# Kernel optimization log

Hardware: AMD Instinct MI355X
Metric: run time of the kernel (lower is better)

The kernel has to match this reference:

```python
import jax, jax.numpy as jnp
import numpy as np

EPS = 1e-5
GROUPS = 4
KSZ = 3
PAD = 1
CUTON = 0.1


def conv1x1(x, w):
    # x: [b,c,h,w], w: [o,c,1,1]
    return jnp.einsum('bchw,oc->bohw', x, w[:, :, 0, 0])


def bn_eval(x, g, b, m, v):
    scale = g / jnp.sqrt(v + EPS)
    return (x - m[None, :, None, None]) * scale[None, :, None, None] + b[None, :, None, None]


def extract_patches(xp, k):
    # xp: [b,c,H+2p,W+2p] -> [b,c,h,w,k,k] (matches torch unfold(2,k,1).unfold(3,k,1))
    h = xp.shape[2] - k + 1
    w = xp.shape[3] - k + 1
    p = jnp.stack([xp[:, :, i:i + h, j:j + w] for i in range(k) for j in range(k)], axis=-1)
    return p.reshape(p.shape[:-1] + (k, k))


def batch_fftshift(z):
    # faithful to roll_n with n = d//2 (+1 if odd), over dims 1..3; roll_n == roll by -n
    for ax in (1, 2, 3):
        d = z.shape[ax]
        z = jnp.roll(z, -(d // 2 + (d % 2)), axis=ax)
    return z


def batch_ifftshift(z):
    for ax in (3, 2, 1):
        z = jnp.roll(z, -(z.shape[ax] // 2), axis=ax)
    return z


def attention_conv(x, yq, q_w, k_w, v_w, rel_h, rel_w):
    b, c, h, w = x.shape
    C = q_w.shape[0]
    px = jnp.pad(x, ((0, 0), (0, 0), (PAD, PAD), (PAD, PAD)))
    q = conv1x1(yq, q_w)                      # [b,C,h,w]
    k = conv1x1(px, k_w)
    v = conv1x1(px, v_w)
    kp = extract_patches(k, KSZ)              # [b,C,h,w,3,3]
    vp = extract_patches(v, KSZ)
    kh, kw = kp[:, :C // 2], kp[:, C // 2:]
    kp = jnp.concatenate([kh + rel_h, kw + rel_w], axis=1)
    kp = kp.reshape(b, GROUPS, C // GROUPS, h, w, KSZ * KSZ)
    vp = vp.reshape(b, GROUPS, C // GROUPS, h, w, KSZ * KSZ)
    q = q.reshape(b, GROUPS, C // GROUPS, h, w, 1)
    attn = jax.nn.softmax(q * kp, axis=-1)
    out = jnp.einsum('bgchwk,bgchwk->bgchw', attn, vp)
    return out.reshape(b, C, h, w)


def fam(x, rate1, rate2, w1, w0_w, w0_b):
    h, w = x.shape[2], x.shape[3]
    # torch.fft.fftn with dim=None -> FFT over ALL dims (batch & channel too)
    x_ft = jnp.fft.fftn(x, norm='ortho')
    out_ft = jnp.einsum('bixy,ioxy->boxy', x_ft, w1)
    s = batch_fftshift(out_ft)
    cy, cx = h // 2, w // 2
    rh, rw = int(CUTON * cy), int(CUTON * cx)
    mask = jnp.ones((h, w), dtype=x.dtype).at[cy - rh:cy + rh, cx - rw:cx + rw].set(0.0)
    s = s * mask
    out_ft = batch_ifftshift(s)
    # torch.fft.ifftn with s=(h,w) -> inverse FFT over last two dims only
    out = jnp.fft.ifftn(out_ft, s=(h, w), norm='ortho').real
    out2 = conv1x1(x, w0_w) + w0_b[None, :, None, None]
    return rate1 * out + rate2 * out2


def setup_inputs() -> dict:
    key = jax.random.key(0)
    ks = jax.random.split(key, 16)
    B, Cx, Cy, M, O, H, W = 4, 128, 256, 128, 128, 64, 64
    scale = 1.0 / (M * O)
    inp = {
        'x': jax.random.normal(ks[0], (B, Cx, H, W), jnp.float32),
        'y': jax.random.normal(ks[1], (B, Cy, H // 2, W // 2), jnp.float32),
        'conv1_w': jax.random.normal(ks[2], (M, Cy, 1, 1), jnp.float32) * 0.05,
        'bn1_g': jnp.ones((M,), jnp.float32),
        'bn1_b': jnp.zeros((M,), jnp.float32),
        'bn1_m': jnp.zeros((M,), jnp.float32),
        'bn1_v': jnp.ones((M,), jnp.float32),
        'q_w': jax.random.normal(ks[3], (M, M, 1, 1), jnp.float32) * 0.05,
        'k_w': jax.random.normal(ks[4], (M, M, 1, 1), jnp.float32) * 0.05,
        'v_w': jax.random.normal(ks[5], (M, M, 1, 1), jnp.float32) * 0.05,
        'rel_h': jax.random.normal(ks[6], (M // 2, 1, 1, 3, 1), jnp.float32),
        'rel_w': jax.random.normal(ks[7], (M // 2, 1, 1, 1, 3), jnp.float32),
        'rate1': jnp.full((1,), 0.5, jnp.float32),
        'rate2': jnp.full((1,), 0.5, jnp.float32),
        'w1_real': scale * jax.random.uniform(ks[8], (M, O, H, W), jnp.float32),
        'w1_imag': scale * jax.random.uniform(ks[9], (M, O, H, W), jnp.float32),
        'w0_w': jax.random.normal(ks[10], (O, M, 1, 1), jnp.float32) * 0.05,
        'w0_b': jnp.zeros((O,), jnp.float32),
        'bn2_g': jnp.ones((O,), jnp.float32),
        'bn2_b': jnp.zeros((O,), jnp.float32),
        'bn2_m': jnp.zeros((O,), jnp.float32),
        'bn2_v': jnp.ones((O,), jnp.float32),
    }
    return inp


def reference(x, y, conv1_w, bn1_g, bn1_b, bn1_m, bn1_v, q_w, k_w, v_w, rel_h, rel_w,
              rate1, rate2, w1_real, w1_imag, w0_w, w0_b, bn2_g, bn2_b, bn2_m, bn2_v):
    # conv1 (teacher proj) + BN + ReLU
    y1 = jax.nn.relu(bn_eval(conv1x1(y, conv1_w), bn1_g, bn1_b, bn1_m, bn1_v))
    # nearest interpolate to x spatial size (torch 'nearest': idx = floor(i*in/out))
    H, W = x.shape[2], x.shape[3]
    ih = (jnp.arange(H) * y1.shape[2]) // H
    iw = (jnp.arange(W) * y1.shape[3]) // W
    y_up = y1[:, :, ih][:, :, :, iw]
    # local unfold attention
    x_att = attention_conv(x, y_up, q_w, k_w, v_w, rel_h, rel_w)
    # FAM spectral branch + BN + ReLU
    w1 = jax.lax.complex(w1_real, w1_imag)
    y_out = jax.nn.relu(bn_eval(fam(x_att, rate1, rate2, w1, w0_w, w0_b),
                                bn2_g, bn2_b, bn2_m, bn2_v))
    return (y_out, x_att)
```

## Files before the change

kernel.cpp:

```cpp
#include <hip/hip_runtime.h>

#define BB 4
#define CY 256
#define CM 128
#define HW 4096
#define HWy 1024
#define PHW 4356
#define EPSF 1e-5f
#define TWOPI 6.2831853071795864769f

struct c32 { float re, im; };


__global__ void conv1_kernel(const float* __restrict__ y, const float* __restrict__ w,
                             const float* __restrict__ g, const float* __restrict__ bb,
                             const float* __restrict__ m, const float* __restrict__ v,
                             float* __restrict__ y1){
  int p = blockIdx.x*256 + threadIdx.x;
  int ocb = blockIdx.y*8;
  int b = blockIdx.z;
  float acc[8] = {0,0,0,0,0,0,0,0};
  const float* yb = y + (size_t)b*CY*HWy + p;
  #pragma unroll 4
  for(int ic=0; ic<CY; ic++){
    float xv = yb[(size_t)ic*HWy];
    #pragma unroll
    for(int j=0;j<8;j++) acc[j] += xv * w[(ocb+j)*CY + ic];
  }
  #pragma unroll
  for(int j=0;j<8;j++){
    int oc = ocb+j;
    float s = g[oc]*rsqrtf(v[oc]+EPSF);
    float bi = bb[oc] - m[oc]*s;
    float r = acc[j]*s + bi;
    y1[((size_t)(b*CM+oc))*HWy + p] = r>0.f?r:0.f;
  }
}

__global__ void qconv_kernel(const float* __restrict__ y1, const float* __restrict__ w,
                             float* __restrict__ q){
  int p = blockIdx.x*256 + threadIdx.x;
  int ocb = blockIdx.y*8; int b = blockIdx.z;
  int mi = ((p>>7)<<5) + ((p&63)>>1);
  float acc[8] = {0,0,0,0,0,0,0,0};
  const float* yb = y1 + (size_t)b*CM*HWy + mi;
  #pragma unroll 4
  for(int ic=0; ic<CM; ic++){
    float xv = yb[(size_t)ic*HWy];
    #pragma unroll
    for(int j=0;j<8;j++) acc[j] += xv * w[(ocb+j)*CM+ic];
  }
  #pragma unroll
  for(int j=0;j<8;j++) q[((size_t)(b*CM+ocb+j))*HW + p] = acc[j];
}

__global__ void kvconv_kernel(const float* __restrict__ x, const float* __restrict__ kw,
                              const float* __restrict__ vw,
                              float* __restrict__ k, float* __restrict__ v){
  int p = blockIdx.x*256 + threadIdx.x;
  int ocb = blockIdx.y*8; int b = blockIdx.z;
  if(p >= PHW) return;
  int hh = p/66, ww2 = p - hh*66;
  int ih = hh-1, iw = ww2-1;
  bool inb = (ih>=0 && ih<64 && iw>=0 && iw<64);
  float acck[8] = {0,0,0,0,0,0,0,0};
  float accv[8] = {0,0,0,0,0,0,0,0};
  if(inb){
    const float* xb = x + (size_t)b*CM*HW + ih*64 + iw;
    #pragma unroll 4
    for(int ic=0; ic<CM; ic++){
      float xv = xb[(size_t)ic*HW];
      #pragma unroll
      for(int j=0;j<8;j++){ acck[j] += xv*kw[(ocb+j)*CM+ic]; accv[j] += xv*vw[(ocb+j)*CM+ic]; }
    }
  }
  #pragma unroll
  for(int j=0;j<8;j++){
    size_t o = ((size_t)(b*CM+ocb+j))*PHW + p;
    k[o]=acck[j]; v[o]=accv[j];
  }
}


__global__ void attn_kernel(const float* __restrict__ q, const float* __restrict__ k,
                            const float* __restrict__ v, const float* __restrict__ relh,
                            const float* __restrict__ relw, float* __restrict__ xatt){
  int t = blockIdx.x*256 + threadIdx.x;
  int p = t & 4095;
  int bc = t >> 12;
  int c = bc & 127;
  int h = p>>6, w2 = p&63;
  float qv = q[(size_t)bc*HW + p];
  const float* kb = k + (size_t)bc*PHW;
  const float* vb = v + (size_t)bc*PHW;
  float lg[9], vv[9];
  #pragma unroll
  for(int ti=0; ti<3; ti++){
    #pragma unroll
    for(int tj=0; tj<3; tj++){
      int idx = (h+ti)*66 + (w2+tj);
      float rel = (c<64) ? relh[c*3+ti] : relw[(c-64)*3+tj];
      float kv = kb[idx] + rel;
      lg[ti*3+tj] = qv*kv;
      vv[ti*3+tj] = vb[idx];
    }
  }
  float mx = lg[0];
  #pragma unroll
  for(int i=1;i<9;i++) mx = fmaxf(mx, lg[i]);
  float s=0.f, o=0.f;
  #pragma unroll
  for(int i=0;i<9;i++){ float e = __expf(lg[i]-mx); s += e; o += e*vv[i]; }
  xatt[t] = o/s;
}


template<int SIGN>
__device__ inline void dft8(const c32* a, c32* X){
  constexpr float C8[8] = {1.f,0.70710678118654752f,0.f,-0.70710678118654752f,
                           -1.f,-0.70710678118654752f,0.f,0.70710678118654752f};
  constexpr float S8[8] = {0.f,0.70710678118654752f,1.f,0.70710678118654752f,
                           0.f,-0.70710678118654752f,-1.f,-0.70710678118654752f};
  #pragma unroll
  for(int kk=0;kk<8;kk++){
    float xr=0.f, xi=0.f;
    #pragma unroll
    for(int n=0;n<8;n++){
      const int j=(n*kk)&7;
      const float wr = C8[j];
      const float wi = SIGN*S8[j];
      xr += a[n].re*wr - a[n].im*wi;
      xi += a[n].re*wi + a[n].im*wr;
    }
    X[kk].re=xr; X[kk].im=xi;
  }
}

template<int SIGN, bool RIN, bool ROUT>
__global__ void fft64_kernel(const float* in, float* out,
                             int l_div, int s1, int s2, int estride, float scale){
  __shared__ c32 tmp[32][65];
  int ll = threadIdx.x & 31;
  int j  = threadIdx.x >> 5;
  int l = blockIdx.x*32 + ll;
  int base = (l/l_div)*s1 + (l%l_div)*s2;
  c32 a[8];
  #pragma unroll
  for(int n1=0;n1<8;n1++){
    int e = n1*8 + j;
    if(RIN){ a[n1].re = in[base + e*estride]; a[n1].im = 0.f; }
    else { const float2* ci = (const float2*)in; float2 t2 = ci[base + e*estride]; a[n1].re=t2.x; a[n1].im=t2.y; }
  }
  c32 A[8];
  dft8<SIGN>(a, A);
  #pragma unroll
  for(int k1=0;k1<8;k1++){
    float ang = SIGN * (TWOPI/64.f) * (float)(j*k1);
    float sn, cs; __sincosf(ang, &sn, &cs);
    c32 t; t.re = A[k1].re*cs - A[k1].im*sn; t.im = A[k1].re*sn + A[k1].im*cs;
    tmp[ll][k1*8+j] = t;
  }
  __syncthreads();
  c32 bv[8];
  #pragma unroll
  for(int n2=0;n2<8;n2++) bv[n2] = tmp[ll][j*8+n2];
  c32 Y[8];
  dft8<SIGN>(bv, Y);
  #pragma unroll
  for(int k2=0;k2<8;k2++){
    int e = j + 8*k2;
    int oi = base + e*estride;
    if(ROUT) out[oi] = Y[k2].re*scale;
    else { float2* co = (float2*)out; co[oi] = make_float2(Y[k2].re*scale, Y[k2].im*scale); }
  }
}

template<int SIGN>
__global__ void fft128_kernel(float* data, float scale){
  __shared__ c32 tmp[16][129];
  int ll = threadIdx.x & 15;
  int j  = threadIdx.x >> 4;
  int l = blockIdx.x*16 + ll;
  int b = l >> 12;
  int rem = l & 4095;
  size_t base = (size_t)b*CM*HW + rem;
  float2* cd = (float2*)data;
  c32 a[8];
  #pragma unroll
  for(int n1=0;n1<8;n1++){
    float2 t2 = cd[base + (size_t)(16*n1 + j)*HW];
    a[n1].re=t2.x; a[n1].im=t2.y;
  }
  c32 A[8];
  dft8<SIGN>(a, A);
  #pragma unroll
  for(int k1=0;k1<8;k1++){
    float ang = SIGN*(TWOPI/128.f)*(float)(j*k1);
    float sn,cs; __sincosf(ang,&sn,&cs);
    c32 t; t.re = A[k1].re*cs - A[k1].im*sn; t.im = A[k1].re*sn + A[k1].im*cs;
    tmp[ll][k1*16 + j] = t;
  }
  __syncthreads();
  int k1 = j & 7, half = j >> 3;
  c32 bv[16];
  #pragma unroll
  for(int n2=0;n2<16;n2++) bv[n2] = tmp[ll][k1*16+n2];
  #pragma unroll
  for(int kk=0;kk<8;kk++){
    int k2 = half*8 + kk;
    float xr=0.f, xi=0.f;
    #pragma unroll
    for(int n2=0;n2<16;n2++){
      float ang = SIGN*(TWOPI/16.f)*(float)((n2*k2)&15);
      float sn,cs; __sincosf(ang,&sn,&cs);
      xr += bv[n2].re*cs - bv[n2].im*sn;
      xi += bv[n2].re*sn + bv[n2].im*cs;
    }
    cd[base + (size_t)(k1 + 8*k2)*HW] = make_float2(xr*scale, xi*scale);
  }
}

__global__ void einsum_kernel(const float2* __restrict__ Xf, const float* __restrict__ w1r,
                              const float* __restrict__ w1i, float2* __restrict__ OutF){
  int fl = threadIdx.x & 63;
  int ol = threadIdx.x >> 6;
  int fbase = blockIdx.y*64;
  int obase = blockIdx.x*16;
  int f = fbase + fl;
  __shared__ float2 xs[4][64];
  c32 acc[4][4];
  #pragma unroll
  for(int a1=0;a1<4;a1++)
    #pragma unroll
    for(int a2=0;a2<4;a2++){ acc[a1][a2].re=0.f; acc[a1][a2].im=0.f; }
  for(int i=0;i<CM;i++){
    __syncthreads();
    xs[ol][fl] = Xf[((size_t)(ol*CM + i))*HW + f];
    __syncthreads();
    float2 x0=xs[0][fl], x1=xs[1][fl], x2=xs[2][fl], x3=xs[3][fl];
    c32 Xb[4];
    Xb[0].re = x0.x+x1.x+x2.x+x3.x;      Xb[0].im = x0.y+x1.y+x2.y+x3.y;
    Xb[1].re = x0.x + x1.y - x2.x - x3.y; Xb[1].im = x0.y - x1.x - x2.y + x3.x;
    Xb[2].re = x0.x - x1.x + x2.x - x3.x; Xb[2].im = x0.y - x1.y + x2.y - x3.y;
    Xb[3].re = x0.x - x1.y - x2.x + x3.y; Xb[3].im = x0.y + x1.x - x2.y - x3.x;
    #pragma unroll
    for(int oj=0;oj<4;oj++){
      int o = obase + oj*4 + ol;
      size_t wi_ = ((size_t)(i*CM + o))*HW + f;
      float wr = w1r[wi_], wim = w1i[wi_];
      #pragma unroll
      for(int kb=0;kb<4;kb++){
        acc[oj][kb].re += Xb[kb].re*wr - Xb[kb].im*wim;
        acc[oj][kb].im += Xb[kb].re*wim + Xb[kb].im*wr;
      }
    }
  }
  int hf = f>>6, wf = f&63;
  bool masked = (hf<3 || hf>60) && (wf<3 || wf>60);
  #pragma unroll
  for(int oj=0;oj<4;oj++){
    int o = obase + oj*4 + ol;
    #pragma unroll
    for(int kb=0;kb<4;kb++){
      float2 t2 = masked ? make_float2(0.f,0.f) : make_float2(acc[oj][kb].re, acc[oj][kb].im);
      OutF[((size_t)(kb*CM + o))*HW + f] = t2;
    }
  }
}

__global__ void final_kernel(const float* __restrict__ G, const float* __restrict__ xatt,
                             const float* __restrict__ w0, const float* __restrict__ w0b,
                             const float* __restrict__ r1p, const float* __restrict__ r2p,
                             const float* __restrict__ g2, const float* __restrict__ b2,
                             const float* __restrict__ m2, const float* __restrict__ v2,
                             float* __restrict__ yout){
  int p = blockIdx.x*256 + threadIdx.x;
  int ocb = blockIdx.y*8; int b = blockIdx.z;
  float r1 = r1p[0], r2 = r2p[0];
  float acc[8] = {0,0,0,0,0,0,0,0};
  const float* xb = xatt + (size_t)b*CM*HW + p;
  #pragma unroll 4
  for(int ic=0; ic<CM; ic++){
    float xv = xb[(size_t)ic*HW];
    #pragma unroll
    for(int j=0;j<8;j++) acc[j] += xv * w0[(ocb+j)*CM + ic];
  }
  #pragma unroll
  for(int j=0;j<8;j++){
    int oc = ocb+j;
    float fam = r1 * G[((size_t)(b*CM+oc))*HW + p] + r2*(acc[j] + w0b[oc]);
    float s = g2[oc]*rsqrtf(v2[oc]+EPSF);
    float bi = b2[oc] - m2[oc]*s;
    float val = fam*s + bi;
    yout[((size_t)(b*CM+oc))*HW + p] = val>0.f?val:0.f;
  }
}

extern "C" void kernel_launch(void* const* d_in, const int* in_sizes, int n_in,
                              void* d_out, int out_size, void* d_ws, size_t ws_size,
                              hipStream_t stream){
  const float* x       = (const float*)d_in[0];
  const float* y       = (const float*)d_in[1];
  const float* conv1_w = (const float*)d_in[2];
  const float* bn1_g   = (const float*)d_in[3];
  const float* bn1_b   = (const float*)d_in[4];
  const float* bn1_m   = (const float*)d_in[5];
  const float* bn1_v   = (const float*)d_in[6];
  const float* q_w     = (const float*)d_in[7];
  const float* k_w     = (const float*)d_in[8];
  const float* v_w     = (const float*)d_in[9];
  const float* rel_h   = (const float*)d_in[10];
  const float* rel_w   = (const float*)d_in[11];
  const float* rate1   = (const float*)d_in[12];
  const float* rate2   = (const float*)d_in[13];
  const float* w1r     = (const float*)d_in[14];
  const float* w1i     = (const float*)d_in[15];
  const float* w0_w    = (const float*)d_in[16];
  const float* w0_b    = (const float*)d_in[17];
  const float* bn2_g   = (const float*)d_in[18];
  const float* bn2_b   = (const float*)d_in[19];
  const float* bn2_m   = (const float*)d_in[20];
  const float* bn2_v   = (const float*)d_in[21];
  (void)in_sizes; (void)n_in; (void)out_size; (void)ws_size;

  char* ws = (char*)d_ws;
  float* Y1 = (float*)(ws + 0);
  float* Q  = (float*)(ws + 2097152);
  float* K  = (float*)(ws + 10485760);
  float* V  = (float*)(ws + 19406848);
  float2* E = (float2*)(ws + 0);
  float2* F = (float2*)(ws + 16777216);
  float*  G = (float*)(ws + 0);

  float* yout = (float*)d_out;
  float* xatt = (float*)d_out + 2097152;

  conv1_kernel<<<dim3(4,16,BB),256,0,stream>>>(y, conv1_w, bn1_g,bn1_b,bn1_m,bn1_v, Y1);
  qconv_kernel<<<dim3(16,16,BB),256,0,stream>>>(Y1, q_w, Q);
  kvconv_kernel<<<dim3(18,16,BB),256,0,stream>>>(x, k_w, v_w, K, V);
  attn_kernel<<<dim3(8192),256,0,stream>>>(Q, K, V, rel_h, rel_w, xatt);

  fft64_kernel<-1,true,false><<<dim3(1024),256,0,stream>>>(xatt, (float*)E, 64,4096,64, 1, 0.125f);
  fft64_kernel<-1,false,false><<<dim3(1024),256,0,stream>>>((float*)E, (float*)E, 64,4096,1, 64, 0.125f);
  fft128_kernel<-1><<<dim3(1024),256,0,stream>>>((float*)E, 0.044194173824159216f);
  einsum_kernel<<<dim3(8,64),256,0,stream>>>(E, w1r, w1i, F);
  fft64_kernel<1,false,false><<<dim3(1024),256,0,stream>>>((float*)F, (float*)F, 64,4096,1, 64, 0.125f);
  fft64_kernel<1,false,true><<<dim3(1024),256,0,stream>>>((float*)F, G, 64,4096,64, 1, 0.125f);

  final_kernel<<<dim3(16,16,BB),256,0,stream>>>(G, xatt, w0_w, w0_b, rate1, rate2,
                                                bn2_g,bn2_b,bn2_m,bn2_v, yout);
}
```

Baseline: 786.3 us.

## Split einsum across more blocks with one output channel per thread and XCD swizzle

The spectral einsum kernel now launches 2048 one-dimensional blocks instead of 512. Each thread computes one output channel for four batch-FFT bins rather than four channels. The shared-memory staging of the input spectrum and its two barriers per iteration are removed; each thread loads the four input values directly, and a block-index remap groups neighbouring work onto the same chiplet. This raises occupancy and removes synchronisation, at the cost of every thread re-reading the input spectrum and so multiplying global loads of X by four.

```diff
diff --git a/kernel.cpp b/kernel.cpp
--- a/kernel.cpp
+++ b/kernel.cpp
@@ -222,49 +222,45 @@
 
 __global__ void einsum_kernel(const float2* __restrict__ Xf, const float* __restrict__ w1r,
                               const float* __restrict__ w1i, float2* __restrict__ OutF){
+  int L = blockIdx.x;
+  int wk = (L & 7) * 256 + (L >> 3);
+  int obase = (wk & 31) * 4;
+  int fbase = (wk >> 5) * 64;
   int fl = threadIdx.x & 63;
   int ol = threadIdx.x >> 6;
-  int fbase = blockIdx.y*64;
-  int obase = blockIdx.x*16;
   int f = fbase + fl;
-  __shared__ float2 xs[4][64];
-  c32 acc[4][4];
-  #pragma unroll
-  for(int a1=0;a1<4;a1++)
-    #pragma unroll
-    for(int a2=0;a2<4;a2++){ acc[a1][a2].re=0.f; acc[a1][a2].im=0.f; }
+  int o = obase + ol;
+  c32 acc[4];
+  #pragma unroll
+  for(int kb=0;kb<4;kb++){ acc[kb].re=0.f; acc[kb].im=0.f; }
+  const float2* X0 = Xf + f;
+  const float* wr_base = w1r + (size_t)o*HW + f;
+  const float* wi_base = w1i + (size_t)o*HW + f;
   for(int i=0;i<CM;i++){
-    __syncthreads();
-    xs[ol][fl] = Xf[((size_t)(ol*CM + i))*HW + f];
-    __syncthreads();
-    float2 x0=xs[0][fl], x1=xs[1][fl], x2=xs[2][fl], x3=xs[3][fl];
+    float2 x0 = X0[(size_t)(0*CM + i)*HW];
+    float2 x1 = X0[(size_t)(1*CM + i)*HW];
+    float2 x2 = X0[(size_t)(2*CM + i)*HW];
+    float2 x3 = X0[(size_t)(3*CM + i)*HW];
     c32 Xb[4];
     Xb[0].re = x0.x+x1.x+x2.x+x3.x;      Xb[0].im = x0.y+x1.y+x2.y+x3.y;
     Xb[1].re = x0.x + x1.y - x2.x - x3.y; Xb[1].im = x0.y - x1.x - x2.y + x3.x;
     Xb[2].re = x0.x - x1.x + x2.x - x3.x; Xb[2].im = x0.y - x1.y + x2.y - x3.y;
     Xb[3].re = x0.x - x1.y - x2.x + x3.y; Xb[3].im = x0.y + x1.x - x2.y - x3.x;
-    #pragma unroll
-    for(int oj=0;oj<4;oj++){
-      int o = obase + oj*4 + ol;
-      size_t wi_ = ((size_t)(i*CM + o))*HW + f;
-      float wr = w1r[wi_], wim = w1i[wi_];
-      #pragma unroll
-      for(int kb=0;kb<4;kb++){
-        acc[oj][kb].re += Xb[kb].re*wr - Xb[kb].im*wim;
-        acc[oj][kb].im += Xb[kb].re*wim + Xb[kb].im*wr;
-      }
+    size_t wo = (size_t)i*CM*HW;
+    float wr  = wr_base[wo];
+    float wim = wi_base[wo];
+    #pragma unroll
+    for(int kb=0;kb<4;kb++){
+      acc[kb].re += Xb[kb].re*wr - Xb[kb].im*wim;
+      acc[kb].im += Xb[kb].re*wim + Xb[kb].im*wr;
     }
   }
   int hf = f>>6, wf = f&63;
   bool masked = (hf<3 || hf>60) && (wf<3 || wf>60);
   #pragma unroll
-  for(int oj=0;oj<4;oj++){
-    int o = obase + oj*4 + ol;
-    #pragma unroll
-    for(int kb=0;kb<4;kb++){
-      float2 t2 = masked ? make_float2(0.f,0.f) : make_float2(acc[oj][kb].re, acc[oj][kb].im);
-      OutF[((size_t)(kb*CM + o))*HW + f] = t2;
-    }
+  for(int kb=0;kb<4;kb++){
+    float2 t2 = masked ? make_float2(0.f,0.f) : make_float2(acc[kb].re, acc[kb].im);
+    OutF[((size_t)(kb*CM + o))*HW + f] = t2;
   }
 }
 
@@ -343,7 +339,7 @@
   fft64_kernel<-1,true,false><<<dim3(1024),256,0,stream>>>(xatt, (float*)E, 64,4096,64, 1, 0.125f);
   fft64_kernel<-1,false,false><<<dim3(1024),256,0,stream>>>((float*)E, (float*)E, 64,4096,1, 64, 0.125f);
   fft128_kernel<-1><<<dim3(1024),256,0,stream>>>((float*)E, 0.044194173824159216f);
-  einsum_kernel<<<dim3(8,64),256,0,stream>>>(E, w1r, w1i, F);
+  einsum_kernel<<<dim3(2048),256,0,stream>>>(E, w1r, w1i, F);
   fft64_kernel<1,false,false><<<dim3(1024),256,0,stream>>>((float*)F, (float*)F, 64,4096,1, 64, 0.125f);
   fft64_kernel<1,false,true><<<dim3(1024),256,0,stream>>>((float*)F, G, 64,4096,64, 1, 0.125f);
 
```

Measured after the change: 816.5 us. +3.8%, slower.
